# Performance work log

Hardware: AMD Instinct MI355X
Metric: run time of the kernel (lower is better)

## Reference

```python
import jax, jax.numpy as jnp
import numpy as np

SEQ, BATCH, HIDDEN = 2048, 2, 1024
NUM_HEADS, HEAD_DIM = 16, 64
LN_EPS = 1e-6
NEG_INF = -1e10


def setup_inputs() -> dict:
    key = jax.random.key(0)
    k1, k2, k3 = jax.random.split(key, 3)
    inputs_q = jax.random.normal(k1, (SEQ, BATCH, HIDDEN), dtype=jnp.float32)
    ln_scale = jnp.ones((HIDDEN,), dtype=jnp.float32)
    ln_bias = jnp.zeros((HIDDEN,), dtype=jnp.float32)
    # fused QKV kernel: (hidden, 3, num_heads*head_dim), fan_in variance scaling
    qkv_kernel = jax.random.normal(k2, (HIDDEN, 3, NUM_HEADS * HEAD_DIM), dtype=jnp.float32) / np.sqrt(HIDDEN).astype(np.float32)
    out_kernel = jax.random.normal(k3, (NUM_HEADS * HEAD_DIM, HIDDEN), dtype=jnp.float32) / np.sqrt(NUM_HEADS * HEAD_DIM).astype(np.float32)
    return {"inputs_q": inputs_q, "ln_scale": ln_scale, "ln_bias": ln_bias,
            "qkv_kernel": qkv_kernel, "out_kernel": out_kernel}


def reference(inputs_q, ln_scale, ln_bias, qkv_kernel, out_kernel):
    s, b, h = inputs_q.shape
    # --- LayerNorm (fused with QKV projection in the original module) ---
    mu = jnp.mean(inputs_q, axis=-1, keepdims=True)
    var = jnp.mean(jnp.square(inputs_q - mu), axis=-1, keepdims=True)
    ln_out = (inputs_q - mu) * jax.lax.rsqrt(var + LN_EPS) * ln_scale + ln_bias
    # --- fused QKV projection: (s,b,h) @ (h,3,nh*hd) -> (s,b,3,nh*hd) ---
    qkv = jnp.einsum('sbh,htk->stbk', ln_out, qkv_kernel)  # (s,3,b,nh*hd)
    q = qkv[:, 0].reshape(s, b, NUM_HEADS, HEAD_DIM)  # (s,b,nh,hd)
    k = qkv[:, 1].reshape(s, b, NUM_HEADS, HEAD_DIM)
    v = qkv[:, 2].reshape(s, b, NUM_HEADS, HEAD_DIM)
    # --- core attention (transpose_batch_sequence=True layout) ---
    scale = 1.0 / np.sqrt(HEAD_DIM).astype(np.float32)  # scale_attn_logits=True
    logits = jnp.einsum('qbhd,kbhd->bhqk', q, k) * scale
    causal = jnp.tril(jnp.ones((s, s), dtype=bool))  # attn_mask_type='causal'
    logits = jnp.where(causal[None, None], logits, jnp.asarray(NEG_INF, logits.dtype))
    attn = jax.nn.softmax(logits, axis=-1)
    ctx = jnp.einsum('bhqk,kbhd->qbhd', attn, v).reshape(s, b, NUM_HEADS * HEAD_DIM)
    # --- output projection ---
    return jnp.einsum('sbk,kh->sbh', ctx, out_kernel)
```

## Files before the change

### kernel.cpp

```cpp
#include <hip/hip_runtime.h>

typedef unsigned short u16;
typedef unsigned int u32;
typedef __attribute__((ext_vector_type(8))) short short8;
typedef __attribute__((ext_vector_type(4))) float f32x4;

#define AS1C(p) ((const __attribute__((address_space(1))) void*)(p))
#define AS3(p)  ((__attribute__((address_space(3))) void*)(p))

constexpr int SEQ = 2048, BATCH = 2, HIDDEN = 1024, NH = 16, HD = 64;
constexpr int MROWS = SEQ * BATCH;
constexpr int QKV_N = 3 * NH * HD;

__device__ __forceinline__ float bf2f(u16 u) {
  union { u32 i; float f; } v; v.i = (u32)u << 16; return v.f;
}
__device__ __forceinline__ u16 f2bf(float f) {
  union { float f; u32 i; } v; v.f = f;
  u32 r = v.i + 0x7fffu + ((v.i >> 16) & 1u);
  return (u16)(r >> 16);
}
__device__ __forceinline__ bool is_f32(const unsigned* probe) { return probe[0] == 0x3F800000u; }

__global__ __launch_bounds__(256) void transpose_k(const void* __restrict__ in,
                                                   u16* __restrict__ out, int R, int C,
                                                   const unsigned* __restrict__ probe) {
  __shared__ alignas(16) u16 t[32][33];
  const bool fm = is_f32(probe);
  int c0 = blockIdx.x * 32, r0 = blockIdx.y * 32;
  int tx = threadIdx.x & 31, ty = threadIdx.x >> 5;
  if (fm) {
    const float* fin = (const float*)in;
#pragma unroll
    for (int i = 0; i < 32; i += 8) t[ty + i][tx] = f2bf(fin[(size_t)(r0 + ty + i) * C + c0 + tx]);
  } else {
    const u16* uin = (const u16*)in;
#pragma unroll
    for (int i = 0; i < 32; i += 8) t[ty + i][tx] = uin[(size_t)(r0 + ty + i) * C + c0 + tx];
  }
  __syncthreads();
#pragma unroll
  for (int i = 0; i < 32; i += 8) out[(size_t)(c0 + ty + i) * R + r0 + tx] = t[tx][ty + i];
}

__global__ __launch_bounds__(256) void ln_k(const void* __restrict__ xv, const void* __restrict__ gv,
                                            const void* __restrict__ bv, u16* __restrict__ y,
                                            const unsigned* __restrict__ probe) {
  const bool fm = is_f32(probe);
  int row = blockIdx.x, t = threadIdx.x;
  float f0, f1, f2, f3, g0, g1, g2, g3, b0, b1, b2, b3;
  if (fm) {
    float4 v = *(const float4*)((const float*)xv + (size_t)row * HIDDEN + t * 4);
    f0 = v.x; f1 = v.y; f2 = v.z; f3 = v.w;
    float4 gg = *(const float4*)((const float*)gv + t * 4);
    g0 = gg.x; g1 = gg.y; g2 = gg.z; g3 = gg.w;
    float4 bb = *(const float4*)((const float*)bv + t * 4);
    b0 = bb.x; b1 = bb.y; b2 = bb.z; b3 = bb.w;
  } else {
    ushort4 v = *(const ushort4*)((const u16*)xv + (size_t)row * HIDDEN + t * 4);
    f0 = bf2f(v.x); f1 = bf2f(v.y); f2 = bf2f(v.z); f3 = bf2f(v.w);
    ushort4 gg = *(const ushort4*)((const u16*)gv + t * 4);
    g0 = bf2f(gg.x); g1 = bf2f(gg.y); g2 = bf2f(gg.z); g3 = bf2f(gg.w);
    ushort4 bb = *(const ushort4*)((const u16*)bv + t * 4);
    b0 = bf2f(bb.x); b1 = bf2f(bb.y); b2 = bf2f(bb.z); b3 = bf2f(bb.w);
  }
  float s = f0 + f1 + f2 + f3;
  float s2 = f0 * f0 + f1 * f1 + f2 * f2 + f3 * f3;
#pragma unroll
  for (int off = 1; off < 64; off <<= 1) { s += __shfl_xor(s, off); s2 += __shfl_xor(s2, off); }
  __shared__ float ps[4], ps2[4];
  int w = t >> 6, lane = t & 63;
  if (lane == 0) { ps[w] = s; ps2[w] = s2; }
  __syncthreads();
  s = ps[0] + ps[1] + ps[2] + ps[3];
  s2 = ps2[0] + ps2[1] + ps2[2] + ps2[3];
  float mu = s * (1.0f / HIDDEN);
  float rstd = rsqrtf(s2 * (1.0f / HIDDEN) - mu * mu + 1e-6f);
  ushort4 o;
  o.x = f2bf((f0 - mu) * rstd * g0 + b0);
  o.y = f2bf((f1 - mu) * rstd * g1 + b1);
  o.z = f2bf((f2 - mu) * rstd * g2 + b2);
  o.w = f2bf((f3 - mu) * rstd * g3 + b3);
  *(ushort4*)(y + (size_t)row * HIDDEN + t * 4) = o;
}

template <int EPI>
__global__ __launch_bounds__(256) void gemm_k(const u16* __restrict__ A, const u16* __restrict__ Bt,
                                              void* __restrict__ o0, u16* __restrict__ o1,
                                              u16* __restrict__ o2, int M, int N, int K,
                                              const unsigned* __restrict__ probe) {
  __shared__ alignas(16) u16 As[128 * 32];
  __shared__ alignas(16) u16 Bs[128 * 32];
  const int bm = blockIdx.x, bn = blockIdx.y;
  const int tid = threadIdx.x, w = tid >> 6, lane = tid & 63;
  const int wr = w >> 1, wc = w & 1, lr = lane & 15, lk = lane >> 4;
  f32x4 acc[4][4] = {};

  for (int k0 = 0; k0 < K; k0 += 32) {
#pragma unroll
    for (int j = 0; j < 2; j++) {
      const int issue = w * 2 + j;
      const int e = issue * 512 + lane * 8;
      const int row = e >> 5, kc = e & 31;
      __builtin_amdgcn_global_load_lds(AS1C(A + (size_t)(bm * 128 + row) * K + k0 + kc),
                                       AS3(As + issue * 512), 16, 0, 0);
      __builtin_amdgcn_global_load_lds(AS1C(Bt + (size_t)(bn * 128 + row) * K + k0 + kc),
                                       AS3(Bs + issue * 512), 16, 0, 0);
    }
    __syncthreads();
    short8 a[4], b[4];
#pragma unroll
    for (int i = 0; i < 4; i++) {
      a[i] = *(const short8*)(As + (wr * 64 + i * 16 + lr) * 32 + lk * 8);
      b[i] = *(const short8*)(Bs + (wc * 64 + i * 16 + lr) * 32 + lk * 8);
    }
#pragma unroll
    for (int mi = 0; mi < 4; mi++)
#pragma unroll
      for (int ni = 0; ni < 4; ni++)
        acc[mi][ni] = __builtin_amdgcn_mfma_f32_16x16x32_bf16(a[mi], b[ni], acc[mi][ni], 0, 0, 0);
    __syncthreads();
  }

  const int r0 = bm * 128 + wr * 64, c0 = bn * 128 + wc * 64;
  if (EPI == 0) {
    const bool fm = is_f32(probe);
#pragma unroll
    for (int mi = 0; mi < 4; mi++)
#pragma unroll
      for (int ni = 0; ni < 4; ni++) {
        int col = c0 + ni * 16 + lr;
#pragma unroll
        for (int j = 0; j < 4; j++) {
          int row = r0 + mi * 16 + lk * 4 + j;
          if (fm) ((float*)o0)[(size_t)row * N + col] = acc[mi][ni][j];
          else    ((u16*)o0)[(size_t)row * N + col] = f2bf(acc[mi][ni][j]);
        }
      }
  } else {
#pragma unroll
    for (int mi = 0; mi < 4; mi++)
#pragma unroll
      for (int ni = 0; ni < 4; ni++) {
        int n = c0 + ni * 16 + lr;
        int t = n >> 10, rem = n & 1023, h = rem >> 6, d = rem & 63;
#pragma unroll
        for (int j = 0; j < 4; j++) {
          int r = r0 + mi * 16 + lk * 4 + j;
          int s = r >> 1, bb = r & 1;
          u16 val = f2bf(acc[mi][ni][j]);
          size_t bh = (size_t)(bb * NH + h);
          if (t == 0)      ((u16*)o0)[(bh * SEQ + s) * HD + d] = val;
          else if (t == 1) o1[(bh * SEQ + s) * HD + d] = val;
          else             o2[(bh * HD + d) * SEQ + s] = val;
        }
      }
  }
}

__global__ __launch_bounds__(256, 3) void attn_k(const u16* __restrict__ Q, const u16* __restrict__ Kb,
                                                 const u16* __restrict__ VT, u16* __restrict__ ctx) {
  const int flat = blockIdx.x;
  const int xu = flat & 7, idx = flat >> 3;
  const int bh = xu * 4 + (idx & 3);
  const int qt = 31 - (idx >> 2);
  const int tid = threadIdx.x;
  const int w = tid >> 6, lane = tid & 63;
  const int lr = lane & 15, lk = lane >> 4;
  const size_t base = (size_t)bh * SEQ * HD;
  const int b = bh >> 4, h = bh & 15;

  __shared__ alignas(16) u16 Ks[2][4096];
  __shared__ alignas(16) u16 Vs[2][4096];
  __shared__ alignas(16) u16 P[4][16 * 72];
  u16* Pw = &P[w][0];
  u32* Pw32 = (u32*)Pw;

  const int st_r = lane >> 3;
  const int st_c = 8 * ((lane & 7) ^ st_r);

  const int qr0 = qt * 64 + w * 16;
  const int qrow = qr0 + lr;
  const int klast = qt;

  short8 aq[2];
#pragma unroll
  for (int kk = 0; kk < 2; kk++)
    aq[kk] = *(const short8*)(Q + base + (size_t)qrow * HD + kk * 32 + lk * 8);

  f32x4 o[4] = {};
  float m = -1e30f, l = 0.0f;

#pragma unroll
  for (int j = 0; j < 2; j++) {
    const int c = j * 4 + w;
    const int r = c * 8 + st_r;
    __builtin_amdgcn_global_load_lds(AS1C(Kb + base + (size_t)r * HD + st_c),
                                     AS3(Ks[0] + c * 512), 16, 0, 0);
    __builtin_amdgcn_global_load_lds(AS1C(VT + base + (size_t)r * SEQ + st_c),
                                     AS3(Vs[0] + c * 512), 16, 0, 0);
  }
  __syncthreads();

  for (int kt = 0; kt <= klast; kt++) {
    const int k0 = kt * 64;
    const int buf = kt & 1;
    if (kt < klast) {
      const int kn = k0 + 64;
#pragma unroll
      for (int j = 0; j < 2; j++) {
        const int c = j * 4 + w;
        const int r = c * 8 + st_r;
        __builtin_amdgcn_global_load_lds(AS1C(Kb + base + (size_t)(kn + r) * HD + st_c),
                                         AS3(Ks[buf ^ 1] + c * 512), 16, 0, 0);
        __builtin_amdgcn_global_load_lds(AS1C(VT + base + (size_t)r * SEQ + kn + st_c),
                                         AS3(Vs[buf ^ 1] + c * 512), 16, 0, 0);
      }
    }
    const int swz = (lr & 7) << 3;
    short8 bk[4][2], bv[4][2];
#pragma unroll
    for (int ni = 0; ni < 4; ni++) {
      const int row = ni * 16 + lr;
#pragma unroll
      for (int kk = 0; kk < 2; kk++)
        bk[ni][kk] = *(const short8*)(Ks[buf] + row * 64 + ((kk * 32 + lk * 8) ^ swz));
#pragma unroll
      for (int ks = 0; ks < 2; ks++)
        bv[ni][ks] = *(const short8*)(Vs[buf] + row * 64 + ((ks * 32 + lk * 8) ^ swz));
    }
    f32x4 s[4] = {};
#pragma unroll
    for (int ni = 0; ni < 4; ni++)
#pragma unroll
      for (int kk = 0; kk < 2; kk++)
        s[ni] = __builtin_amdgcn_mfma_f32_16x16x32_bf16(bk[ni][kk], aq[kk], s[ni], 0, 0, 0);
#pragma unroll
    for (int ni = 0; ni < 4; ni++)
#pragma unroll
      for (int j = 0; j < 4; j++) {
        float v = s[ni][j] * 0.125f;
        if (kt == klast) {
          if (k0 + ni * 16 + lk * 4 + j > qrow) v = -1e30f;
        }
        s[ni][j] = v;
      }
    float pm = s[0][0];
#pragma unroll
    for (int ni = 0; ni < 4; ni++)
#pragma unroll
      for (int j = 0; j < 4; j++) pm = fmaxf(pm, s[ni][j]);
    pm = fmaxf(pm, __shfl_xor(pm, 16));
    pm = fmaxf(pm, __shfl_xor(pm, 32));
    const float nm = fmaxf(m, pm);
    const float fac = __expf(m - nm);
    float rs = 0.0f;
#pragma unroll
    for (int ni = 0; ni < 4; ni++)
#pragma unroll
      for (int j = 0; j < 4; j++) {
        float p = __expf(s[ni][j] - nm);
        s[ni][j] = p;
        rs += p;
      }
    rs += __shfl_xor(rs, 16);
    rs += __shfl_xor(rs, 32);
    l = l * fac + rs;
    m = nm;
#pragma unroll
    for (int ni = 0; ni < 4; ni++) {
      uint2 pk;
      pk.x = (u32)f2bf(s[ni][0]) | ((u32)f2bf(s[ni][1]) << 16);
      pk.y = (u32)f2bf(s[ni][2]) | ((u32)f2bf(s[ni][3]) << 16);
      *(uint2*)(Pw32 + lr * 36 + ni * 8 + lk * 2) = pk;
    }
    short8 pa[2];
#pragma unroll
    for (int kk = 0; kk < 2; kk++)
      pa[kk] = *(const short8*)(Pw + lr * 72 + kk * 32 + lk * 8);
    float f0 = __shfl(fac, lk * 4 + 0);
    float f1 = __shfl(fac, lk * 4 + 1);
    float f2 = __shfl(fac, lk * 4 + 2);
    float f3 = __shfl(fac, lk * 4 + 3);
#pragma unroll
    for (int ni = 0; ni < 4; ni++) {
      o[ni][0] *= f0; o[ni][1] *= f1; o[ni][2] *= f2; o[ni][3] *= f3;
    }
#pragma unroll
    for (int ni = 0; ni < 4; ni++)
#pragma unroll
      for (int kk = 0; kk < 2; kk++)
        o[ni] = __builtin_amdgcn_mfma_f32_16x16x32_bf16(pa[kk], bv[ni][kk], o[ni], 0, 0, 0);
    __syncthreads();
  }
  float linv0 = 1.0f / __shfl(l, lk * 4 + 0);
  float linv1 = 1.0f / __shfl(l, lk * 4 + 1);
  float linv2 = 1.0f / __shfl(l, lk * 4 + 2);
  float linv3 = 1.0f / __shfl(l, lk * 4 + 3);
#pragma unroll
  for (int ni = 0; ni < 4; ni++) {
    int col = h * HD + ni * 16 + lr;
    ctx[(size_t)((qr0 + lk * 4 + 0) * BATCH + b) * (NH * HD) + col] = f2bf(o[ni][0] * linv0);
    ctx[(size_t)((qr0 + lk * 4 + 1) * BATCH + b) * (NH * HD) + col] = f2bf(o[ni][1] * linv1);
    ctx[(size_t)((qr0 + lk * 4 + 2) * BATCH + b) * (NH * HD) + col] = f2bf(o[ni][2] * linv2);
    ctx[(size_t)((qr0 + lk * 4 + 3) * BATCH + b) * (NH * HD) + col] = f2bf(o[ni][3] * linv3);
  }
}

extern "C" void kernel_launch(void* const* d_in, const int* in_sizes, int n_in,
                              void* d_out, int out_size, void* d_ws, size_t ws_size,
                              hipStream_t stream) {
  const void* x    = d_in[0];
  const void* g    = d_in[1];
  const void* bta  = d_in[2];
  const void* wqkv = d_in[3];
  const void* wout = d_in[4];
  const unsigned* probe = (const unsigned*)d_in[1];

  char* ws = (char*)d_ws;
  u16* ln   = (u16*)(ws);
  u16* q    = (u16*)(ws + 8388608);
  u16* k    = (u16*)(ws + 16777216);
  u16* vT   = (u16*)(ws + 25165824);
  u16* qkvT = (u16*)(ws + 33554432);
  u16* outT = (u16*)(ws + 33554432 + 6291456);
  u16* ctx  = ln;

  transpose_k<<<dim3(QKV_N / 32, HIDDEN / 32), 256, 0, stream>>>(wqkv, qkvT, HIDDEN, QKV_N, probe);
  transpose_k<<<dim3(HIDDEN / 32, HIDDEN / 32), 256, 0, stream>>>(wout, outT, HIDDEN, HIDDEN, probe);
  ln_k<<<MROWS, 256, 0, stream>>>(x, g, bta, ln, probe);
  gemm_k<1><<<dim3(MROWS / 128, QKV_N / 128), 256, 0, stream>>>(ln, qkvT, q, k, vT,
                                                                MROWS, QKV_N, HIDDEN, probe);
  attn_k<<<dim3(1024), 256, 0, stream>>>(q, k, vT, ctx);
  gemm_k<0><<<dim3(MROWS / 128, HIDDEN / 128), 256, 0, stream>>>(ctx, outT, d_out, nullptr, nullptr,
                                                                 MROWS, HIDDEN, HIDDEN, probe);
}
```

Baseline: 131.1 us.

## Swizzle GEMM LDS tiles, remap blocks across XCDs, stage QKV epilogue through LDS

```diff
diff --git a/kernel.cpp b/kernel.cpp
--- a/kernel.cpp
+++ b/kernel.cpp
@@ -88,31 +88,37 @@
 __global__ __launch_bounds__(256) void gemm_k(const u16* __restrict__ A, const u16* __restrict__ Bt,
                                               void* __restrict__ o0, u16* __restrict__ o1,
                                               u16* __restrict__ o2, int M, int N, int K,
-                                              const unsigned* __restrict__ probe) {
+                                              const unsigned* __restrict__ probe, int nbm) {
   __shared__ alignas(16) u16 As[128 * 32];
   __shared__ alignas(16) u16 Bs[128 * 32];
-  const int bm = blockIdx.x, bn = blockIdx.y;
+  const int g = gridDim.x;
+  const int wg = (blockIdx.x & 7) * (g >> 3) + (blockIdx.x >> 3);
+  const int bm = wg % nbm, bn = wg / nbm;
   const int tid = threadIdx.x, w = tid >> 6, lane = tid & 63;
   const int wr = w >> 1, wc = w & 1, lr = lane & 15, lk = lane >> 4;
   f32x4 acc[4][4] = {};
 
+  const int srow_lo = lane >> 2;
+  const int sslot = lane & 3;
+  const int csw = ((lk ^ ((lr >> 1) & 3)) * 8);
+
   for (int k0 = 0; k0 < K; k0 += 32) {
 #pragma unroll
     for (int j = 0; j < 2; j++) {
       const int issue = w * 2 + j;
-      const int e = issue * 512 + lane * 8;
-      const int row = e >> 5, kc = e & 31;
-      __builtin_amdgcn_global_load_lds(AS1C(A + (size_t)(bm * 128 + row) * K + k0 + kc),
-                                       AS3(As + issue * 512), 16, 0, 0);
-      __builtin_amdgcn_global_load_lds(AS1C(Bt + (size_t)(bn * 128 + row) * K + k0 + kc),
-                                       AS3(Bs + issue * 512), 16, 0, 0);
+      const int row = issue * 16 + srow_lo;
+      const int src = ((sslot ^ ((row >> 1) & 3)) * 8);
+      __builtin_amdgcn_global_load_lds(AS1C(A + (size_t)(bm * 128 + row) * K + k0 + src),
+                                       AS3(As + issue * 512 + lane * 8), 16, 0, 0);
+      __builtin_amdgcn_global_load_lds(AS1C(Bt + (size_t)(bn * 128 + row) * K + k0 + src),
+                                       AS3(Bs + issue * 512 + lane * 8), 16, 0, 0);
     }
     __syncthreads();
     short8 a[4], b[4];
 #pragma unroll
     for (int i = 0; i < 4; i++) {
-      a[i] = *(const short8*)(As + (wr * 64 + i * 16 + lr) * 32 + lk * 8);
-      b[i] = *(const short8*)(Bs + (wc * 64 + i * 16 + lr) * 32 + lk * 8);
+      a[i] = *(const short8*)(As + (wr * 64 + i * 16 + lr) * 32 + csw);
+      b[i] = *(const short8*)(Bs + (wc * 64 + i * 16 + lr) * 32 + csw);
     }
 #pragma unroll
     for (int mi = 0; mi < 4; mi++)
@@ -122,8 +128,8 @@
     __syncthreads();
   }
 
-  const int r0 = bm * 128 + wr * 64, c0 = bn * 128 + wc * 64;
-  if (EPI == 0) {
+  if constexpr (EPI == 0) {
+    const int r0 = bm * 128 + wr * 64, c0 = bn * 128 + wc * 64;
     const bool fm = is_f32(probe);
 #pragma unroll
     for (int mi = 0; mi < 4; mi++)
@@ -138,23 +144,56 @@
         }
       }
   } else {
-#pragma unroll
-    for (int mi = 0; mi < 4; mi++)
-#pragma unroll
-      for (int ni = 0; ni < 4; ni++) {
-        int n = c0 + ni * 16 + lr;
-        int t = n >> 10, rem = n & 1023, h = rem >> 6, d = rem & 63;
-#pragma unroll
-        for (int j = 0; j < 4; j++) {
-          int r = r0 + mi * 16 + lk * 4 + j;
-          int s = r >> 1, bb = r & 1;
-          u16 val = f2bf(acc[mi][ni][j]);
-          size_t bh = (size_t)(bb * NH + h);
-          if (t == 0)      ((u16*)o0)[(bh * SEQ + s) * HD + d] = val;
-          else if (t == 1) o1[(bh * SEQ + s) * HD + d] = val;
-          else             o2[(bh * HD + d) * SEQ + s] = val;
-        }
-      }
+    __shared__ alignas(16) u16 E[9216];
+    const int t = bn >> 3;
+    u16* q = (u16*)o0;
+#pragma unroll
+    for (int p = 0; p < 2; p++) {
+      if (wc == p) {
+        if (t < 2) {
+#pragma unroll
+          for (int mi = 0; mi < 4; mi++)
+#pragma unroll
+            for (int ni = 0; ni < 4; ni++)
+#pragma unroll
+              for (int j = 0; j < 4; j++)
+                E[(wr * 64 + mi * 16 + lk * 4 + j) * 72 + ni * 16 + lr] = f2bf(acc[mi][ni][j]);
+        } else {
+#pragma unroll
+          for (int mi = 0; mi < 4; mi++)
+#pragma unroll
+            for (int ni = 0; ni < 4; ni++)
+#pragma unroll
+              for (int j = 0; j < 4; j++) {
+                int r = wr * 64 + mi * 16 + lk * 4 + j;
+                E[(r & 1) * 4608 + (ni * 16 + lr) * 72 + (r >> 1)] = f2bf(acc[mi][ni][j]);
+              }
+        }
+      }
+      __syncthreads();
+      const int h = ((bn & 7) * 2) + p;
+      if (t < 2) {
+        u16* dst = (t == 0) ? q : o1;
+#pragma unroll
+        for (int st = 0; st < 4; st++) {
+          int row = st * 32 + (tid >> 3);
+          int d8 = (tid & 7) * 8;
+          short8 v = *(const short8*)(E + row * 72 + d8);
+          int gr = bm * 128 + row, s = gr >> 1, bb = gr & 1;
+          *(short8*)(dst + (((size_t)(bb * NH + h) * SEQ + s) * HD + d8)) = v;
+        }
+      } else {
+#pragma unroll
+        for (int st = 0; st < 4; st++) {
+          int row = st * 32 + (tid >> 3);
+          int bb = row >> 6, d = row & 63;
+          int s8 = (tid & 7) * 8;
+          short8 v = *(const short8*)(E + bb * 4608 + d * 72 + s8);
+          *(short8*)(o2 + ((size_t)((bb * NH + h) * HD + d) * SEQ + bm * 64 + s8)) = v;
+        }
+      }
+      __syncthreads();
+    }
   }
 }
 
@@ -329,9 +368,11 @@
   transpose_k<<<dim3(QKV_N / 32, HIDDEN / 32), 256, 0, stream>>>(wqkv, qkvT, HIDDEN, QKV_N, probe);
   transpose_k<<<dim3(HIDDEN / 32, HIDDEN / 32), 256, 0, stream>>>(wout, outT, HIDDEN, HIDDEN, probe);
   ln_k<<<MROWS, 256, 0, stream>>>(x, g, bta, ln, probe);
-  gemm_k<1><<<dim3(MROWS / 128, QKV_N / 128), 256, 0, stream>>>(ln, qkvT, q, k, vT,
-                                                                MROWS, QKV_N, HIDDEN, probe);
+  gemm_k<1><<<dim3((MROWS / 128) * (QKV_N / 128)), 256, 0, stream>>>(ln, qkvT, q, k, vT,
+                                                                     MROWS, QKV_N, HIDDEN, probe,
+                                                                     MROWS / 128);
   attn_k<<<dim3(1024), 256, 0, stream>>>(q, k, vT, ctx);
-  gemm_k<0><<<dim3(MROWS / 128, HIDDEN / 128), 256, 0, stream>>>(ctx, outT, d_out, nullptr, nullptr,
-                                                                 MROWS, HIDDEN, HIDDEN, probe);
-}
+  gemm_k<0><<<dim3((MROWS / 128) * (HIDDEN / 128)), 256, 0, stream>>>(ctx, outT, d_out, nullptr,
+                                                                      nullptr, MROWS, HIDDEN,
+                                                                      HIDDEN, probe, MROWS / 128);
+}
```

Result: slower. 141.5 us (+8.0%).
